# Performance work log

Hardware: AMD Instinct MI355X
Metric: run time of the kernel (lower is better)

## Reference

```python
import jax, jax.numpy as jnp
import numpy as np

MODEL_DIM = 1024
NUM_HEADS = 16
D_K = MODEL_DIM // NUM_HEADS  # 64
MAX_SEQ_LEN = 3200
B, T = 2, 2048
THETA_BASE = 10000.0


def setup_inputs() -> dict:
    key = jax.random.key(0)
    ks = jax.random.split(key, 5)
    scale = 1.0 / np.sqrt(MODEL_DIM)
    x = jax.random.normal(ks[0], (B, T, MODEL_DIM), dtype=jnp.float32)
    wq = jax.random.normal(ks[1], (MODEL_DIM, MODEL_DIM), dtype=jnp.float32) * scale
    wk = jax.random.normal(ks[2], (MODEL_DIM, MODEL_DIM), dtype=jnp.float32) * scale
    wv = jax.random.normal(ks[3], (MODEL_DIM, MODEL_DIM), dtype=jnp.float32) * scale
    wo = jax.random.normal(ks[4], (MODEL_DIM, MODEL_DIM), dtype=jnp.float32) * scale
    bq = jnp.zeros((MODEL_DIM,), jnp.float32)
    bk = jnp.zeros((MODEL_DIM,), jnp.float32)
    bv = jnp.zeros((MODEL_DIM,), jnp.float32)
    bo = jnp.zeros((MODEL_DIM,), jnp.float32)
    # RoPE tables, exactly as precompute_rotation_matrix: theta duplicated
    # adjacently ([t0,t0,t1,t1,...]).
    theta = THETA_BASE ** (jnp.arange(D_K // 2, dtype=jnp.float32) * (-2.0 / D_K))
    ang = jnp.outer(jnp.arange(MAX_SEQ_LEN, dtype=jnp.float32), theta)  # [L, d/2]
    ang = jnp.repeat(ang, 2, axis=-1)  # [L, d]
    return {
        "x": x, "wq": wq, "bq": bq, "wk": wk, "bk": bk,
        "wv": wv, "bv": bv, "wo": wo, "bo": bo,
        "cos": jnp.cos(ang), "sin": jnp.sin(ang),
    }


def reference(x, wq, bq, wk, bk, wv, bv, wo, bo, cos, sin):
    b, t, dm = x.shape
    h, d = NUM_HEADS, dm // NUM_HEADS

    # NOTE: original uses .view(b, h, t, d) directly on [b, t, h*d] (no
    # transpose) — a nonstandard head split we replicate faithfully.
    xq = (x @ wq.T + bq).reshape(b, h, t, d)
    xk = (x @ wk.T + bk).reshape(b, h, t, d)
    xv = (x @ wv.T + bv).reshape(b, h, t, d)

    def rot_half(q):
        # pairs are adjacent (2i, 2i+1): out[2i] = -q[2i+1], out[2i+1] = q[2i]
        q2 = q.reshape(b, h, t, d // 2, 2)
        return jnp.stack([-q2[..., 1], q2[..., 0]], axis=-1).reshape(b, h, t, d)

    # NOTE: original indexes cos/sin at the single position `seq_len`
    # (rotation_matrix_cos[:, :, xq.shape[2], :]), broadcasting one row over
    # all positions — replicated faithfully.
    c = cos[t]  # [d]
    s = sin[t]  # [d]
    xq = xq * c + rot_half(xq) * s
    xk = xk * c + rot_half(xk) * s

    scores = jnp.einsum("bhqd,bhkd->bhqk", xq, xk) / np.sqrt(d)
    p = jax.nn.softmax(scores, axis=-1)  # mask='none', dropout=0.0
    o = jnp.einsum("bhqk,bhkd->bhqd", p, xv)
    o = o.transpose(0, 2, 1, 3).reshape(b, t, dm)  # 'b h t d -> b t (h d)'
    return o @ wo.T + bo
```

## Files before the change

kernel.cpp:

```cpp
#include <hip/hip_runtime.h>

typedef _Float16 half8 __attribute__((ext_vector_type(8)));
typedef float floatx4 __attribute__((ext_vector_type(4)));


__global__ __launch_bounds__(256) void convert_kernel(
    const float* __restrict__ x, const float* __restrict__ wq,
    const float* __restrict__ wk, const float* __restrict__ wv,
    const float* __restrict__ wo,
    _Float16* __restrict__ xb, _Float16* __restrict__ wqkv,
    _Float16* __restrict__ wob)
{
    int i = (blockIdx.x * 256 + threadIdx.x) * 4;
    const float* src; _Float16* dst; int off;
    if (i < 4194304)      { src = x;  dst = xb;            off = i; }
    else if (i < 5242880) { src = wq; dst = wqkv;          off = i - 4194304; }
    else if (i < 6291456) { src = wk; dst = wqkv + 1048576; off = i - 5242880; }
    else if (i < 7340032) { src = wv; dst = wqkv + 2097152; off = i - 6291456; }
    else                  { src = wo; dst = wob;           off = i - 7340032; }
    float4 v = *(const float4*)(src + off);
    union { uint2 u; _Float16 h[4]; } o;
    o.h[0] = (_Float16)v.x; o.h[1] = (_Float16)v.y;
    o.h[2] = (_Float16)v.z; o.h[3] = (_Float16)v.w;
    *(uint2*)(dst + off) = o.u;
}

template<bool QKV>
__global__ __launch_bounds__(256) void gemm_kernel(
    const _Float16* __restrict__ A, const _Float16* __restrict__ W,
    const float* __restrict__ b0, const float* __restrict__ b1,
    const float* __restrict__ b2,
    const float* __restrict__ cosr, const float* __restrict__ sinr,
    _Float16* __restrict__ O0, _Float16* __restrict__ O1,
    _Float16* __restrict__ O2, float* __restrict__ Of)
{
    __shared__ __align__(16) _Float16 As[128][72];
    __shared__ __align__(16) _Float16 Bs[128][72];
    const int tid  = threadIdx.x;
    const int lane = tid & 63, w = tid >> 6;
    const int lrow = lane & 15, quad = lane >> 4;
    const int mblk = blockIdx.x, nblk = blockIdx.y;
    const int wr = (w & 1) * 64, wc = (w >> 1) * 64;
    const int arow0 = mblk * 128;
    const int brow0 = nblk * 128;

    floatx4 acc[4][4] = {};

    for (int kk = 0; kk < 1024; kk += 64) {
        for (int i = 0; i < 4; i++) {
            int c = tid + i * 256;
            int row = c >> 3, col8 = (c & 7) * 8;
            *(uint4*)&As[row][col8] = *(const uint4*)(A + (arow0 + row) * 1024 + kk + col8);
            *(uint4*)&Bs[row][col8] = *(const uint4*)(W + (brow0 + row) * 1024 + kk + col8);
        }
        __syncthreads();
        for (int ks = 0; ks < 2; ks++) {
            half8 af[4], bf[4];
            for (int mt = 0; mt < 4; mt++)
                af[mt] = *(const half8*)&As[wr + mt * 16 + lrow][ks * 32 + quad * 8];
            for (int nt = 0; nt < 4; nt++)
                bf[nt] = *(const half8*)&Bs[wc + nt * 16 + lrow][ks * 32 + quad * 8];
            for (int mt = 0; mt < 4; mt++)
                for (int nt = 0; nt < 4; nt++)
                    acc[mt][nt] = __builtin_amdgcn_mfma_f32_16x16x32_f16(
                        af[mt], bf[nt], acc[mt][nt], 0, 0, 0);
        }
        __syncthreads();
    }

    if (QKV) {
        const int seg = nblk >> 3;
        const float* bias = seg == 0 ? b0 : (seg == 1 ? b1 : b2);
        _Float16* out = seg == 0 ? O0 : (seg == 1 ? O1 : O2);
        const int nbase = (nblk & 7) * 128 + wc;
        for (int nt = 0; nt < 4; nt++) {
            const int n = nbase + nt * 16 + lrow;
            const float bv = bias[n];
            const int dj = n & 63;
            const float cv = cosr[dj], sv = sinr[dj];
            const bool odd = (n & 1) != 0;
            for (int mt = 0; mt < 4; mt++)
                for (int r = 0; r < 4; r++) {
                    float v = acc[mt][nt][r] + bv;
                    if (seg < 2) {
                        float p = __shfl_xor(v, 1, 64);
                        v = odd ? (v * cv + p * sv) : (v * cv - p * sv);
                    }
                    if (seg == 0) v *= 0.125f;
                    int row = arow0 + wr + mt * 16 + quad * 4 + r;
                    out[row * 1024 + n] = (_Float16)v;
                }
        }
    } else {
        const int nbase = nblk * 128 + wc;
        for (int nt = 0; nt < 4; nt++) {
            const int n = nbase + nt * 16 + lrow;
            const float bv = b0[n];
            for (int mt = 0; mt < 4; mt++)
                for (int r = 0; r < 4; r++) {
                    int row = arow0 + wr + mt * 16 + quad * 4 + r;
                    Of[row * 1024 + n] = acc[mt][nt][r] + bv;
                }
        }
    }
}

__global__ __launch_bounds__(256, 3) void attn_kernel(
    const _Float16* __restrict__ Q, const _Float16* __restrict__ K,
    const _Float16* __restrict__ V, _Float16* __restrict__ O)
{
    __shared__ __align__(16) _Float16 Ks[2][64][72];
    __shared__ __align__(16) _Float16 Vts[2][64][72];
    __shared__ __align__(16) _Float16 Pt[4][32][40];

    const int tid  = threadIdx.x;
    const int lane = tid & 63, w = tid >> 6;
    const int lrow = lane & 15, quad = lane >> 4;
    const int qt = blockIdx.x, bh = blockIdx.y;
    const int bi = bh >> 4, hi = bh & 15;
    const size_t base = (size_t)(bi * 2048 + hi * 128) * 1024;
    const _Float16* Qh = Q + base;
    const _Float16* Kh = K + base;
    const _Float16* Vh = V + base;

    half8 qf[2][2];
    for (int nt = 0; nt < 2; nt++)
        for (int ks = 0; ks < 2; ks++)
            qf[nt][ks] = *(const half8*)(Qh + (qt * 128 + w * 32 + nt * 16 + lrow) * 64
                                          + ks * 32 + quad * 8);

    floatx4 oacc[4][2] = {};
    float lsum0 = 0.0f, lsum1 = 0.0f;

    const int srow = tid >> 3, sblk = tid & 7;
    const int ckey = (2 * srow) ^ (sblk * 8);

    {
        uint4 k0 = *(const uint4*)(Kh + srow * 64 + sblk * 8);
        uint4 k1 = *(const uint4*)(Kh + (srow + 32) * 64 + sblk * 8);
        uint4 v0 = *(const uint4*)(Vh + (2 * srow) * 64 + sblk * 8);
        uint4 v1 = *(const uint4*)(Vh + (2 * srow + 1) * 64 + sblk * 8);
        *(uint4*)&Ks[0][srow][sblk * 8]      = k0;
        *(uint4*)&Ks[0][srow + 32][sblk * 8] = k1;
        union { uint4 u; _Float16 h[8]; } a, b;
        a.u = v0; b.u = v1;
        for (int j = 0; j < 8; j++) {
            union { unsigned u; _Float16 h[2]; } pk;
            pk.h[0] = a.h[j]; pk.h[1] = b.h[j];
            *(unsigned*)&Vts[0][sblk * 8 + j][ckey] = pk.u;
        }
    }
    __syncthreads();

    for (int kt = 0; kt < 32; kt++) {
        const int cur = kt & 1;
        uint4 k0, k1, v0, v1;
        if (kt < 31) {
            const _Float16* Kt = Kh + (kt + 1) * 4096;
            const _Float16* Vt = Vh + (kt + 1) * 4096;
            k0 = *(const uint4*)(Kt + srow * 64 + sblk * 8);
            k1 = *(const uint4*)(Kt + (srow + 32) * 64 + sblk * 8);
            v0 = *(const uint4*)(Vt + (2 * srow) * 64 + sblk * 8);
            v1 = *(const uint4*)(Vt + (2 * srow + 1) * 64 + sblk * 8);
        }
        for (int h = 0; h < 2; h++) {
            for (int k2 = 0; k2 < 2; k2++) {
                const int kt4 = h * 2 + k2;
                floatx4 s0 = {}, s1 = {};
                for (int ks = 0; ks < 2; ks++) {
                    half8 af = *(const half8*)&Ks[cur][kt4 * 16 + lrow][ks * 32 + quad * 8];
                    s0 = __builtin_amdgcn_mfma_f32_16x16x32_f16(af, qf[0][ks], s0, 0, 0, 0);
                    s1 = __builtin_amdgcn_mfma_f32_16x16x32_f16(af, qf[1][ks], s1, 0, 0, 0);
                }
                union { uint2 u; _Float16 h4[4]; } pk0, pk1;
                for (int r = 0; r < 4; r++) {
                    float p0 = exp2f(fmaf(s0[r], 1.44269504f, -8.65617025f));
                    float p1 = exp2f(fmaf(s1[r], 1.44269504f, -8.65617025f));
                    lsum0 += p0; lsum1 += p1;
                    pk0.h4[r] = (_Float16)p0; pk1.h4[r] = (_Float16)p1;
                }
                *(uint2*)&Pt[w][lrow][k2 * 16 + quad * 4]      = pk0.u;
                *(uint2*)&Pt[w][16 + lrow][k2 * 16 + quad * 4] = pk1.u;
            }
            half8 bf0 = *(const half8*)&Pt[w][lrow][quad * 8];
            half8 bf1 = *(const half8*)&Pt[w][16 + lrow][quad * 8];
            for (int dt = 0; dt < 4; dt++) {
                const int blk = ((h * 4 + quad) ^ (2 * dt + (lrow >> 3))) & 7;
                half8 av = *(const half8*)&Vts[cur][dt * 16 + lrow][blk * 8];
                oacc[dt][0] = __builtin_amdgcn_mfma_f32_16x16x32_f16(av, bf0, oacc[dt][0], 0, 0, 0);
                oacc[dt][1] = __builtin_amdgcn_mfma_f32_16x16x32_f16(av, bf1, oacc[dt][1], 0, 0, 0);
            }
        }
        if (kt < 31) {
            const int nxt = cur ^ 1;
            *(uint4*)&Ks[nxt][srow][sblk * 8]      = k0;
            *(uint4*)&Ks[nxt][srow + 32][sblk * 8] = k1;
            union { uint4 u; _Float16 h[8]; } a, b;
            a.u = v0; b.u = v1;
            for (int j = 0; j < 8; j++) {
                union { unsigned u; _Float16 h[2]; } pk;
                pk.h[0] = a.h[j]; pk.h[1] = b.h[j];
                *(unsigned*)&Vts[nxt][sblk * 8 + j][ckey] = pk.u;
            }
        }
        __syncthreads();
    }

    lsum0 += __shfl_xor(lsum0, 16, 64); lsum0 += __shfl_xor(lsum0, 32, 64);
    lsum1 += __shfl_xor(lsum1, 16, 64); lsum1 += __shfl_xor(lsum1, 32, 64);
    const float inv0 = 1.0f / lsum0, inv1 = 1.0f / lsum1;
    _Float16* Es = (_Float16*)Ks + w * 2304;
    for (int dt = 0; dt < 4; dt++) {
        union { uint2 u; _Float16 h[4]; } a0, a1;
        for (int r = 0; r < 4; r++) {
            a0.h[r] = (_Float16)(oacc[dt][0][r] * inv0);
            a1.h[r] = (_Float16)(oacc[dt][1][r] * inv1);
        }
        *(uint2*)&Es[lrow * 72 + dt * 16 + quad * 4]        = a0.u;
        *(uint2*)&Es[(16 + lrow) * 72 + dt * 16 + quad * 4] = a1.u;
    }
    const int rw = lane >> 1, hf = lane & 1;
    const size_t orow = (size_t)(bi * 2048 + qt * 128 + w * 32 + rw) * 1024
                        + hi * 64 + hf * 32;
    for (int i = 0; i < 4; i++)
        *(uint4*)(O + orow + i * 8) = *(const uint4*)&Es[rw * 72 + hf * 32 + i * 8];
}

extern "C" void kernel_launch(void* const* d_in, const int* in_sizes, int n_in,
                              void* d_out, int out_size, void* d_ws, size_t ws_size,
                              hipStream_t stream) {
    const float* x    = (const float*)d_in[0];
    const float* wq   = (const float*)d_in[1];
    const float* bq   = (const float*)d_in[2];
    const float* wk   = (const float*)d_in[3];
    const float* bk   = (const float*)d_in[4];
    const float* wv   = (const float*)d_in[5];
    const float* bv   = (const float*)d_in[6];
    const float* wo   = (const float*)d_in[7];
    const float* bo   = (const float*)d_in[8];
    const float* cosT = (const float*)d_in[9];
    const float* sinT = (const float*)d_in[10];

    _Float16* ws   = (_Float16*)d_ws;
    _Float16* xb   = ws;
    _Float16* wqkv = xb + 4194304;
    _Float16* wob  = wqkv + 3145728;
    _Float16* Qb   = wob + 1048576;
    _Float16* Kb   = Qb + 4194304;
    _Float16* Vb   = Kb + 4194304;
    _Float16* Ob   = Vb + 4194304;

    convert_kernel<<<8192, 256, 0, stream>>>(x, wq, wk, wv, wo, xb, wqkv, wob);
    gemm_kernel<true><<<dim3(32, 24), 256, 0, stream>>>(
        xb, wqkv, bq, bk, bv, cosT + 2048 * 64, sinT + 2048 * 64,
        Qb, Kb, Vb, nullptr);
    attn_kernel<<<dim3(16, 32), 256, 0, stream>>>(Qb, Kb, Vb, Ob);
    gemm_kernel<false><<<dim3(32, 8), 256, 0, stream>>>(
        Ob, wob, bo, nullptr, nullptr, nullptr, nullptr,
        nullptr, nullptr, nullptr, (float*)d_out);
}
```

Measured before the change: 226.7 us.

## Use direct global-to-LDS loads in GEMM, pre-transpose V, fast exp/packed converts

```diff
diff --git a/kernel.cpp b/kernel.cpp
--- a/kernel.cpp
+++ b/kernel.cpp
@@ -1,7 +1,11 @@
 #include <hip/hip_runtime.h>
 
 typedef _Float16 half8 __attribute__((ext_vector_type(8)));
+typedef __fp16 pkh2 __attribute__((ext_vector_type(2)));
 typedef float floatx4 __attribute__((ext_vector_type(4)));
+
+#define AS1 __attribute__((address_space(1)))
+#define AS3 __attribute__((address_space(3)))
 
 
 __global__ __launch_bounds__(256) void convert_kernel(
@@ -19,9 +23,9 @@
     else if (i < 7340032) { src = wv; dst = wqkv + 2097152; off = i - 6291456; }
     else                  { src = wo; dst = wob;           off = i - 7340032; }
     float4 v = *(const float4*)(src + off);
-    union { uint2 u; _Float16 h[4]; } o;
-    o.h[0] = (_Float16)v.x; o.h[1] = (_Float16)v.y;
-    o.h[2] = (_Float16)v.z; o.h[3] = (_Float16)v.w;
+    union { uint2 u; pkh2 h[2]; } o;
+    o.h[0] = __builtin_amdgcn_cvt_pkrtz(v.x, v.y);
+    o.h[1] = __builtin_amdgcn_cvt_pkrtz(v.z, v.w);
     *(uint2*)(dst + off) = o.u;
 }
 
@@ -34,45 +38,51 @@
     _Float16* __restrict__ O0, _Float16* __restrict__ O1,
     _Float16* __restrict__ O2, float* __restrict__ Of)
 {
-    __shared__ __align__(16) _Float16 As[128][72];
-    __shared__ __align__(16) _Float16 Bs[128][72];
+    __shared__ __align__(16) _Float16 As[128 * 64];
+    __shared__ __align__(16) _Float16 Bs[128 * 64];
     const int tid  = threadIdx.x;
     const int lane = tid & 63, w = tid >> 6;
     const int lrow = lane & 15, quad = lane >> 4;
-    const int mblk = blockIdx.x, nblk = blockIdx.y;
     const int wr = (w & 1) * 64, wc = (w >> 1) * 64;
-    const int arow0 = mblk * 128;
-    const int brow0 = nblk * 128;
+    const int arow0 = blockIdx.x * 128;
+    const int brow0 = blockIdx.y * 128;
+
+    const int r8 = lane >> 3;
+    const int gcol = ((lane & 7) ^ r8) * 8;
 
     floatx4 acc[4][4] = {};
 
     for (int kk = 0; kk < 1024; kk += 64) {
-        for (int i = 0; i < 4; i++) {
-            int c = tid + i * 256;
-            int row = c >> 3, col8 = (c & 7) * 8;
-            *(uint4*)&As[row][col8] = *(const uint4*)(A + (arow0 + row) * 1024 + kk + col8);
-            *(uint4*)&Bs[row][col8] = *(const uint4*)(W + (brow0 + row) * 1024 + kk + col8);
+        __syncthreads();
+        for (int u = 0; u < 4; u++) {
+            const int row = w * 32 + u * 8;
+            __builtin_amdgcn_global_load_lds(
+                (const AS1 unsigned*)(const void*)(A + (size_t)(arow0 + row + r8) * 1024 + kk + gcol),
+                (AS3 unsigned*)(void*)(As + row * 64), 16, 0, 0);
+            __builtin_amdgcn_global_load_lds(
+                (const AS1 unsigned*)(const void*)(W + (size_t)(brow0 + row + r8) * 1024 + kk + gcol),
+                (AS3 unsigned*)(void*)(Bs + row * 64), 16, 0, 0);
         }
         __syncthreads();
         for (int ks = 0; ks < 2; ks++) {
+            const int swz = ((ks * 4 + quad) ^ (lrow & 7)) * 8;
             half8 af[4], bf[4];
             for (int mt = 0; mt < 4; mt++)
-                af[mt] = *(const half8*)&As[wr + mt * 16 + lrow][ks * 32 + quad * 8];
+                af[mt] = *(const half8*)&As[(wr + mt * 16 + lrow) * 64 + swz];
             for (int nt = 0; nt < 4; nt++)
-                bf[nt] = *(const half8*)&Bs[wc + nt * 16 + lrow][ks * 32 + quad * 8];
+                bf[nt] = *(const half8*)&Bs[(wc + nt * 16 + lrow) * 64 + swz];
             for (int mt = 0; mt < 4; mt++)
                 for (int nt = 0; nt < 4; nt++)
                     acc[mt][nt] = __builtin_amdgcn_mfma_f32_16x16x32_f16(
                         af[mt], bf[nt], acc[mt][nt], 0, 0, 0);
         }
-        __syncthreads();
     }
 
     if (QKV) {
-        const int seg = nblk >> 3;
+        const int seg = blockIdx.y >> 3;
         const float* bias = seg == 0 ? b0 : (seg == 1 ? b1 : b2);
         _Float16* out = seg == 0 ? O0 : (seg == 1 ? O1 : O2);
-        const int nbase = (nblk & 7) * 128 + wc;
+        const int nbase = (blockIdx.y & 7) * 128 + wc;
         for (int nt = 0; nt < 4; nt++) {
             const int n = nbase + nt * 16 + lrow;
             const float bv = bias[n];
@@ -92,7 +102,7 @@
                 }
         }
     } else {
-        const int nbase = nblk * 128 + wc;
+        const int nbase = blockIdx.y * 128 + wc;
         for (int nt = 0; nt < 4; nt++) {
             const int n = nbase + nt * 16 + lrow;
             const float bv = b0[n];
@@ -105,9 +115,34 @@
     }
 }
 
+__global__ __launch_bounds__(256) void vtrans_kernel(
+    const _Float16* __restrict__ V, _Float16* __restrict__ VT)
+{
+    __shared__ __align__(16) _Float16 T[64][72];
+    const int tid = threadIdx.x;
+    const int kt = blockIdx.x;
+    const int bh = blockIdx.y;
+    const int bi = bh >> 4, hi = bh & 15;
+    const _Float16* Vh = V + (size_t)(bi * 2048 + hi * 128) * 1024 + kt * 4096;
+    const int srow = tid >> 3, sblk = tid & 7;
+    union { uint4 u; _Float16 h[8]; } a, b;
+    a.u = *(const uint4*)(Vh + (2 * srow) * 64 + sblk * 8);
+    b.u = *(const uint4*)(Vh + (2 * srow + 1) * 64 + sblk * 8);
+    for (int j = 0; j < 8; j++) {
+        union { unsigned u; _Float16 h[2]; } pk;
+        pk.h[0] = a.h[j]; pk.h[1] = b.h[j];
+        *(unsigned*)&T[sblk * 8 + j][2 * srow] = pk.u;
+    }
+    __syncthreads();
+    const int d = tid >> 2, c = tid & 3;
+    _Float16* out = VT + ((size_t)bh * 64 + d) * 2048 + kt * 64 + c * 16;
+    *(uint4*)(out)     = *(const uint4*)&T[d][c * 16];
+    *(uint4*)(out + 8) = *(const uint4*)&T[d][c * 16 + 8];
+}
+
 __global__ __launch_bounds__(256, 3) void attn_kernel(
     const _Float16* __restrict__ Q, const _Float16* __restrict__ K,
-    const _Float16* __restrict__ V, _Float16* __restrict__ O)
+    const _Float16* __restrict__ VT, _Float16* __restrict__ O)
 {
     __shared__ __align__(16) _Float16 Ks[2][64][72];
     __shared__ __align__(16) _Float16 Vts[2][64][72];
@@ -119,9 +154,9 @@
     const int qt = blockIdx.x, bh = blockIdx.y;
     const int bi = bh >> 4, hi = bh & 15;
     const size_t base = (size_t)(bi * 2048 + hi * 128) * 1024;
-    const _Float16* Qh = Q + base;
-    const _Float16* Kh = K + base;
-    const _Float16* Vh = V + base;
+    const _Float16* Qh  = Q + base;
+    const _Float16* Kh  = K + base;
+    const _Float16* VTh = VT + (size_t)bh * 131072;
 
     half8 qf[2][2];
     for (int nt = 0; nt < 2; nt++)
@@ -133,35 +168,30 @@
     float lsum0 = 0.0f, lsum1 = 0.0f;
 
     const int srow = tid >> 3, sblk = tid & 7;
-    const int ckey = (2 * srow) ^ (sblk * 8);
+    const int vd = tid >> 2, vc = tid & 3;
 
     {
-        uint4 k0 = *(const uint4*)(Kh + srow * 64 + sblk * 8);
-        uint4 k1 = *(const uint4*)(Kh + (srow + 32) * 64 + sblk * 8);
-        uint4 v0 = *(const uint4*)(Vh + (2 * srow) * 64 + sblk * 8);
-        uint4 v1 = *(const uint4*)(Vh + (2 * srow + 1) * 64 + sblk * 8);
-        *(uint4*)&Ks[0][srow][sblk * 8]      = k0;
-        *(uint4*)&Ks[0][srow + 32][sblk * 8] = k1;
-        union { uint4 u; _Float16 h[8]; } a, b;
-        a.u = v0; b.u = v1;
-        for (int j = 0; j < 8; j++) {
-            union { unsigned u; _Float16 h[2]; } pk;
-            pk.h[0] = a.h[j]; pk.h[1] = b.h[j];
-            *(unsigned*)&Vts[0][sblk * 8 + j][ckey] = pk.u;
-        }
+        *(uint4*)&Ks[0][srow][sblk * 8]      = *(const uint4*)(Kh + srow * 64 + sblk * 8);
+        *(uint4*)&Ks[0][srow + 32][sblk * 8] = *(const uint4*)(Kh + (srow + 32) * 64 + sblk * 8);
+        const _Float16* vsrc = VTh + (size_t)vd * 2048 + vc * 16;
+        *(uint4*)&Vts[0][vd][vc * 16]     = *(const uint4*)(vsrc);
+        *(uint4*)&Vts[0][vd][vc * 16 + 8] = *(const uint4*)(vsrc + 8);
     }
     __syncthreads();
+
+    const float LOG2E = 1.44269504f;
+    const float OFF   = -8.65617025f;
 
     for (int kt = 0; kt < 32; kt++) {
         const int cur = kt & 1;
         uint4 k0, k1, v0, v1;
         if (kt < 31) {
             const _Float16* Kt = Kh + (kt + 1) * 4096;
-            const _Float16* Vt = Vh + (kt + 1) * 4096;
+            const _Float16* Vt = VTh + (size_t)vd * 2048 + (kt + 1) * 64 + vc * 16;
             k0 = *(const uint4*)(Kt + srow * 64 + sblk * 8);
             k1 = *(const uint4*)(Kt + (srow + 32) * 64 + sblk * 8);
-            v0 = *(const uint4*)(Vt + (2 * srow) * 64 + sblk * 8);
-            v1 = *(const uint4*)(Vt + (2 * srow + 1) * 64 + sblk * 8);
+            v0 = *(const uint4*)(Vt);
+            v1 = *(const uint4*)(Vt + 8);
         }
         for (int h = 0; h < 2; h++) {
             for (int k2 = 0; k2 < 2; k2++) {
@@ -172,21 +202,28 @@
                     s0 = __builtin_amdgcn_mfma_f32_16x16x32_f16(af, qf[0][ks], s0, 0, 0, 0);
                     s1 = __builtin_amdgcn_mfma_f32_16x16x32_f16(af, qf[1][ks], s1, 0, 0, 0);
                 }
-                union { uint2 u; _Float16 h4[4]; } pk0, pk1;
-                for (int r = 0; r < 4; r++) {
-                    float p0 = exp2f(fmaf(s0[r], 1.44269504f, -8.65617025f));
-                    float p1 = exp2f(fmaf(s1[r], 1.44269504f, -8.65617025f));
-                    lsum0 += p0; lsum1 += p1;
-                    pk0.h4[r] = (_Float16)p0; pk1.h4[r] = (_Float16)p1;
-                }
+                float p00 = __builtin_amdgcn_exp2f(fmaf(s0[0], LOG2E, OFF));
+                float p01 = __builtin_amdgcn_exp2f(fmaf(s0[1], LOG2E, OFF));
+                float p02 = __builtin_amdgcn_exp2f(fmaf(s0[2], LOG2E, OFF));
+                float p03 = __builtin_amdgcn_exp2f(fmaf(s0[3], LOG2E, OFF));
+                float p10 = __builtin_amdgcn_exp2f(fmaf(s1[0], LOG2E, OFF));
+                float p11 = __builtin_amdgcn_exp2f(fmaf(s1[1], LOG2E, OFF));
+                float p12 = __builtin_amdgcn_exp2f(fmaf(s1[2], LOG2E, OFF));
+                float p13 = __builtin_amdgcn_exp2f(fmaf(s1[3], LOG2E, OFF));
+                lsum0 += p00 + p01 + p02 + p03;
+                lsum1 += p10 + p11 + p12 + p13;
+                union { uint2 u; pkh2 h2[2]; } pk0, pk1;
+                pk0.h2[0] = __builtin_amdgcn_cvt_pkrtz(p00, p01);
+                pk0.h2[1] = __builtin_amdgcn_cvt_pkrtz(p02, p03);
+                pk1.h2[0] = __builtin_amdgcn_cvt_pkrtz(p10, p11);
+                pk1.h2[1] = __builtin_amdgcn_cvt_pkrtz(p12, p13);
                 *(uint2*)&Pt[w][lrow][k2 * 16 + quad * 4]      = pk0.u;
                 *(uint2*)&Pt[w][16 + lrow][k2 * 16 + quad * 4] = pk1.u;
             }
             half8 bf0 = *(const half8*)&Pt[w][lrow][quad * 8];
             half8 bf1 = *(const half8*)&Pt[w][16 + lrow][quad * 8];
             for (int dt = 0; dt < 4; dt++) {
-                const int blk = ((h * 4 + quad) ^ (2 * dt + (lrow >> 3))) & 7;
-                half8 av = *(const half8*)&Vts[cur][dt * 16 + lrow][blk * 8];
+                half8 av = *(const half8*)&Vts[cur][dt * 16 + lrow][h * 32 + quad * 8];
                 oacc[dt][0] = __builtin_amdgcn_mfma_f32_16x16x32_f16(av, bf0, oacc[dt][0], 0, 0, 0);
                 oacc[dt][1] = __builtin_amdgcn_mfma_f32_16x16x32_f16(av, bf1, oacc[dt][1], 0, 0, 0);
             }
@@ -195,13 +232,8 @@
             const int nxt = cur ^ 1;
             *(uint4*)&Ks[nxt][srow][sblk * 8]      = k0;
             *(uint4*)&Ks[nxt][srow + 32][sblk * 8] = k1;
-            union { uint4 u; _Float16 h[8]; } a, b;
-            a.u = v0; b.u = v1;
-            for (int j = 0; j < 8; j++) {
-                union { unsigned u; _Float16 h[2]; } pk;
-                pk.h[0] = a.h[j]; pk.h[1] = b.h[j];
-                *(unsigned*)&Vts[nxt][sblk * 8 + j][ckey] = pk.u;
-            }
+            *(uint4*)&Vts[nxt][vd][vc * 16]     = v0;
+            *(uint4*)&Vts[nxt][vd][vc * 16 + 8] = v1;
         }
         __syncthreads();
     }
@@ -211,11 +243,11 @@
     const float inv0 = 1.0f / lsum0, inv1 = 1.0f / lsum1;
     _Float16* Es = (_Float16*)Ks + w * 2304;
     for (int dt = 0; dt < 4; dt++) {
-        union { uint2 u; _Float16 h[4]; } a0, a1;
-        for (int r = 0; r < 4; r++) {
-            a0.h[r] = (_Float16)(oacc[dt][0][r] * inv0);
-            a1.h[r] = (_Float16)(oacc[dt][1][r] * inv1);
-        }
+        union { uint2 u; pkh2 h2[2]; } a0, a1;
+        a0.h2[0] = __builtin_amdgcn_cvt_pkrtz(oacc[dt][0][0] * inv0, oacc[dt][0][1] * inv0);
+        a0.h2[1] = __builtin_amdgcn_cvt_pkrtz(oacc[dt][0][2] * inv0, oacc[dt][0][3] * inv0);
+        a1.h2[0] = __builtin_amdgcn_cvt_pkrtz(oacc[dt][1][0] * inv1, oacc[dt][1][1] * inv1);
+        a1.h2[1] = __builtin_amdgcn_cvt_pkrtz(oacc[dt][1][2] * inv1, oacc[dt][1][3] * inv1);
         *(uint2*)&Es[lrow * 72 + dt * 16 + quad * 4]        = a0.u;
         *(uint2*)&Es[(16 + lrow) * 72 + dt * 16 + quad * 4] = a1.u;
     }
@@ -249,12 +281,14 @@
     _Float16* Kb   = Qb + 4194304;
     _Float16* Vb   = Kb + 4194304;
     _Float16* Ob   = Vb + 4194304;
+    _Float16* VTb  = xb;
 
     convert_kernel<<<8192, 256, 0, stream>>>(x, wq, wk, wv, wo, xb, wqkv, wob);
     gemm_kernel<true><<<dim3(32, 24), 256, 0, stream>>>(
         xb, wqkv, bq, bk, bv, cosT + 2048 * 64, sinT + 2048 * 64,
         Qb, Kb, Vb, nullptr);
-    attn_kernel<<<dim3(16, 32), 256, 0, stream>>>(Qb, Kb, Vb, Ob);
+    vtrans_kernel<<<dim3(32, 32), 256, 0, stream>>>(Vb, VTb);
+    attn_kernel<<<dim3(16, 32), 256, 0, stream>>>(Qb, Kb, VTb, Ob);
     gemm_kernel<false><<<dim3(32, 8), 256, 0, stream>>>(
         Ob, wob, bo, nullptr, nullptr, nullptr, nullptr,
         nullptr, nullptr, nullptr, (float*)d_out);
```

New measurement: 217.7 us. 1.04x faster.
